# Optimization experiments

Hardware: AMD Instinct MI355X
Metric: run time of the kernel (lower is better)

## Reference

```python
import jax, jax.numpy as jnp
import numpy as np

COMMITMENT_COST = 0.25


def setup_inputs() -> dict:
    key = jax.random.key(0)
    k1, k2 = jax.random.split(key)
    B, H, W, D, K = 64, 32, 32, 64, 1024
    x = jax.random.normal(k1, (B, H, W, D), dtype=jnp.float32)
    # variance_scaling(fan_in=D, uniform) ~ U(-sqrt(3/D), sqrt(3/D)); plain normal*scale is fine for a reference
    embeddings = jax.random.uniform(k2, (D, K), dtype=jnp.float32,
                                    minval=-np.sqrt(3.0 / D), maxval=np.sqrt(3.0 / D))
    return {"x": x, "embeddings": embeddings}


def reference(x, embeddings):
    D = embeddings.shape[0]
    K = embeddings.shape[1]
    flat = x.reshape(-1, D)                                   # [N, D]
    # squared euclidean distance: ||f||^2 - 2 f.E + ||e||^2 -> [N, K]
    distance = (jnp.sum(flat ** 2, axis=1, keepdims=True)
                - 2.0 * jnp.matmul(flat, embeddings)
                + jnp.sum(embeddings ** 2, axis=0, keepdims=True))
    encoding_indices_flat = jnp.argmax(-distance, axis=1)     # [N]
    encodings = jax.nn.one_hot(encoding_indices_flat, K, dtype=distance.dtype)  # [N, K]
    encoding_indices = encoding_indices_flat.reshape(x.shape[:-1])
    # quantize: gather rows of E^T -> same shape as x
    quantized = jnp.take(embeddings.T, encoding_indices, axis=0)
    e_latent_loss = jnp.mean((jax.lax.stop_gradient(quantized) - x) ** 2)
    q_latent_loss = jnp.mean((quantized - jax.lax.stop_gradient(x)) ** 2)
    loss = q_latent_loss + COMMITMENT_COST * e_latent_loss
    quantized_st = x + jax.lax.stop_gradient(quantized - x)   # straight-through
    avg_probs = jnp.mean(encodings, axis=0)                   # [K]
    perplexity = jnp.exp(-jnp.sum(avg_probs * jnp.log(avg_probs + 1e-10)))
    return quantized_st, loss, perplexity, encoding_indices
```

## Files before the change

kernel.cpp:

```cpp
#include <hip/hip_runtime.h>
#include <math.h>


typedef __attribute__((ext_vector_type(8))) short short8v;
typedef __attribute__((ext_vector_type(4))) float float4v;
typedef unsigned short u16;
typedef unsigned int u32;

constexpr int D = 64;
constexpr int K = 1024;
constexpr int NPTS = 65536;
constexpr long QOFF = (long)NPTS * D;
constexpr float BIAS = 24.0f;
constexpr float GATE = 5e-3f;

constexpr size_t OFF_LOSS = 0;
constexpr size_t OFF_CNT  = 256;
constexpr size_t OFF_EC   = OFF_CNT + 4096;
constexpr size_t OFF_ECB  = OFF_EC + 4096;
constexpr size_t OFF_ET   = OFF_ECB + 4096;
constexpr size_t OFF_STG  = OFF_ET + (size_t)K * D * 4;

__device__ __forceinline__ float med3(float a, float b, float c) {
  return __builtin_amdgcn_fmed3f(a, b, c);
}
__device__ __forceinline__ u16 bf16rtn(float x) {
  u32 u = __float_as_uint(x);
  return (u16)((u + 0x7fffu + ((u >> 16) & 1u)) >> 16);
}
__device__ __forceinline__ float bf2f(u16 h) {
  return __uint_as_float(((u32)h) << 16);
}
__device__ __forceinline__ void gl_lds16(const void* g, void* l) {
  __builtin_amdgcn_global_load_lds(
      (const __attribute__((address_space(1))) u32*)g,
      (__attribute__((address_space(3))) u32*)l, 16, 0, 0);
}

__global__ __launch_bounds__(256) void vq_prep(const float* __restrict__ E,
                                               float* __restrict__ eC,
                                               float* __restrict__ eCb,
                                               float* __restrict__ Et,
                                               unsigned char* __restrict__ stg,
                                               double* __restrict__ lossSum,
                                               int* __restrict__ counts) {
  const int b = blockIdx.x;
  const int tid = threadIdx.x;
  if (b < 32) {
    int gid = b * 256 + tid;
    int k = gid & 1023;
    int g = gid >> 10;
    float v[8];
#pragma unroll
    for (int j = 0; j < 8; ++j) v[j] = E[(g * 8 + j) * K + k];
    *(float4*)&Et[(size_t)k * 64 + g * 8] = make_float4(v[0], v[1], v[2], v[3]);
    *(float4*)&Et[(size_t)k * 64 + g * 8 + 4] = make_float4(v[4], v[5], v[6], v[7]);
    short8v hv, lv;
#pragma unroll
    for (int j = 0; j < 8; ++j) {
      float m2 = -2.0f * v[j];
      u16 h = bf16rtn(m2);
      hv[j] = (short)h;
      lv[j] = (short)bf16rtn(m2 - bf2f(h));
    }
    size_t rowb = (size_t)(k >> 7) * 32768 + (size_t)(k & 127) * 256;
    int s = g >> 2, q = g & 3;
    int off = (s * 64 + q * 16) ^ ((k & 7) * 16);
    *(short8v*)&stg[rowb + off] = hv;
    *(short8v*)&stg[rowb + 128 + off] = lv;
  } else {
    int k = (b - 32) * 256 + tid;
    float c = __fmul_rn(E[k], E[k]);
#pragma unroll
    for (int d = 1; d < D; ++d) {
      float vv = E[d * K + k];
      c = __fadd_rn(c, __fmul_rn(vv, vv));
    }
    eC[k] = c;
    eCb[k] = c + BIAS;
    counts[k] = 0;
    if (k == 0) *lossSum = 0.0;
  }
}

__global__ __launch_bounds__(256) void vq_main(const float* __restrict__ x,
                                               const unsigned char* __restrict__ stg,
                                               const float* __restrict__ eC,
                                               const float* __restrict__ eCb,
                                               const float* __restrict__ Etg,
                                               float* __restrict__ out,
                                               double* __restrict__ lossSum,
                                               int* __restrict__ counts) {
  __shared__ __align__(16) unsigned char sbuf[2][32768];
  __shared__ __align__(16) float ecb[1024];
  __shared__ __align__(16) float topbuf[256 * 4];
  __shared__ int bkbuf[128];

  const int tid = threadIdx.x;
  const int w = tid >> 6;
  const int lane = tid & 63;
  const int col = lane & 15;
  const int quad = lane >> 4;
  const int blockBase = blockIdx.x * 128;
  const float INF = __builtin_inff();

  *(float4*)&ecb[tid * 4] = *(const float4*)&eCb[tid * 4];

  short8v Bh[2][2], Bl[2][2];
#pragma unroll
  for (int pt = 0; pt < 2; ++pt) {
    const float* xp = x + (size_t)(blockBase + w * 32 + pt * 16 + col) * 64;
#pragma unroll
    for (int s = 0; s < 2; ++s) {
      const float4* src = (const float4*)(xp + s * 32 + quad * 8);
      float4 a = src[0], b = src[1];
      float xs[8] = {a.x, a.y, a.z, a.w, b.x, b.y, b.z, b.w};
      short8v hf, lf;
#pragma unroll
      for (int j = 0; j < 8; ++j) {
        u16 h = bf16rtn(xs[j]);
        hf[j] = (short)h;
        lf[j] = (short)bf16rtn(xs[j] - bf2f(h));
      }
      Bh[pt][s] = hf;
      Bl[pt][s] = lf;
    }
  }

  {
    const unsigned char* s0 = stg + (size_t)tid * 16;
#pragma unroll
    for (int i = 0; i < 8; ++i)
      gl_lds16(s0 + i * 4096, &sbuf[0][tid * 16 + i * 4096]);
#pragma unroll
    for (int i = 0; i < 8; ++i)
      gl_lds16(s0 + 32768 + i * 4096, &sbuf[1][tid * 16 + i * 4096]);
  }
  asm volatile("s_waitcnt vmcnt(8) lgkmcnt(0)" ::: "memory");
  __builtin_amdgcn_s_barrier();
  __builtin_amdgcn_sched_barrier(0);
  asm volatile("" ::: "memory");

  float b1[2] = {INF, INF}, b2[2] = {INF, INF};
  const int swz = (col & 7) * 16;

#pragma unroll 1
  for (int ch = 0; ch < 8; ++ch) {
    unsigned char* bufB = sbuf[ch & 1];
#pragma unroll
    for (int ct = 0; ct < 8; ++ct) {
      const int rb = ct * 4096 + col * 256;
      short8v Ah0 = *(const short8v*)&bufB[rb + ((quad * 16) ^ swz)];
      short8v Ah1 = *(const short8v*)&bufB[rb + ((64 + quad * 16) ^ swz)];
      short8v Al0 = *(const short8v*)&bufB[rb + 128 + ((quad * 16) ^ swz)];
      short8v Al1 = *(const short8v*)&bufB[rb + 128 + ((64 + quad * 16) ^ swz)];
      float4v Ci = *(const float4v*)&ecb[ch * 128 + ct * 16 + quad * 4];
#pragma unroll
      for (int pt = 0; pt < 2; ++pt) {
        float4v Ca = Ci;
        float4v Cb = {0.f, 0.f, 0.f, 0.f};
        Ca = __builtin_amdgcn_mfma_f32_16x16x32_bf16(Ah0, Bh[pt][0], Ca, 0, 0, 0);
        Cb = __builtin_amdgcn_mfma_f32_16x16x32_bf16(Ah1, Bh[pt][1], Cb, 0, 0, 0);
        Ca = __builtin_amdgcn_mfma_f32_16x16x32_bf16(Al0, Bh[pt][0], Ca, 0, 0, 0);
        Cb = __builtin_amdgcn_mfma_f32_16x16x32_bf16(Al1, Bh[pt][1], Cb, 0, 0, 0);
        Ca = __builtin_amdgcn_mfma_f32_16x16x32_bf16(Ah0, Bl[pt][0], Ca, 0, 0, 0);
        Cb = __builtin_amdgcn_mfma_f32_16x16x32_bf16(Ah1, Bl[pt][1], Cb, 0, 0, 0);
#pragma unroll
        for (int r = 0; r < 4; ++r) {
          float dv = Ca[r] + Cb[r];
          u32 u = (__float_as_uint(dv) & 0xffffff00u) |
                  (u32)(ch * 32 + ct * 4 + r);
          float v = __uint_as_float(u);
          float pb = b1[pt];
          b1[pt] = fminf(pb, v);
          b2[pt] = med3(pb, b2[pt], v);
        }
      }
    }
    asm volatile("s_waitcnt lgkmcnt(0)" ::: "memory");
    __builtin_amdgcn_s_barrier();
    __builtin_amdgcn_sched_barrier(0);
    asm volatile("" ::: "memory");
    if (ch < 6) {
      const unsigned char* s2 = stg + (size_t)(ch + 2) * 32768 + (size_t)tid * 16;
#pragma unroll
      for (int i = 0; i < 8; ++i)
        gl_lds16(s2 + i * 4096, &bufB[tid * 16 + i * 4096]);
      asm volatile("s_waitcnt vmcnt(8)" ::: "memory");
    } else if (ch == 6) {
      asm volatile("s_waitcnt vmcnt(0)" ::: "memory");
    }
    if (ch < 7) {
      __builtin_amdgcn_s_barrier();
      __builtin_amdgcn_sched_barrier(0);
      asm volatile("" ::: "memory");
    }
  }

  topbuf[tid * 4 + 0] = b1[0];
  topbuf[tid * 4 + 1] = b2[0];
  topbuf[tid * 4 + 2] = b1[1];
  topbuf[tid * 4 + 3] = b2[1];
  __syncthreads();

  if (tid < 128) {
    const int mw = tid >> 5, mpt = (tid >> 4) & 1, mcol = tid & 15;
    float cv[8];
    int cq[8];
    float mv0 = INF, mv1 = INF;
    int q0 = 0;
#pragma unroll
    for (int q = 0; q < 4; ++q) {
      int lbase = (mw * 64 + q * 16 + mcol) * 4 + mpt * 2;
#pragma unroll
      for (int j = 0; j < 2; ++j) {
        float v = topbuf[lbase + j];
        cv[q * 2 + j] = v;
        cq[q * 2 + j] = q;
        if (v < mv0) { mv1 = mv0; mv0 = v; q0 = q; }
        else if (v < mv1) { mv1 = v; }
      }
    }
    u32 lb = __float_as_uint(mv0) & 255u;
    int bestk = (int)((lb >> 5) * 128 + ((lb >> 2) & 7) * 16 + q0 * 4 + (lb & 3));

    if (mv1 - mv0 < GATE) {
      const float* f = x + (size_t)(blockBase + tid) * 64;
      float r8[8];
#pragma unroll
      for (int j = 0; j < 8; ++j) { float fv = f[j]; r8[j] = __fmul_rn(fv, fv); }
#pragma unroll
      for (int i = 8; i < D; i += 8)
#pragma unroll
        for (int j = 0; j < 8; ++j) {
          float fv = f[i + j];
          r8[j] = __fadd_rn(r8[j], __fmul_rn(fv, fv));
        }
      float A = __fadd_rn(__fadd_rn(__fadd_rn(r8[0], r8[1]), __fadd_rn(r8[2], r8[3])),
                          __fadd_rn(__fadd_rn(r8[4], r8[5]), __fadd_rn(r8[6], r8[7])));
      float bd = INF;
      int bkk = K;
#pragma unroll
      for (int c = 0; c < 8; ++c) {
        u32 cb = __float_as_uint(cv[c]) & 255u;
        int k = (int)((cb >> 5) * 128 + ((cb >> 2) & 7) * 16 + cq[c] * 4 + (cb & 3));
        const float* er = Etg + (size_t)k * 64;
        float m = 0.f;
#pragma unroll
        for (int d = 0; d < D; ++d) m = __fmaf_rn(f[d], er[d], m);
        float dist = __fadd_rn(__fsub_rn(A, __fmul_rn(2.f, m)), eC[k]);
        bool better = (dist < bd) || (dist == bd && k < bkk);
        bd = better ? dist : bd;
        bkk = better ? k : bkk;
      }
      bestk = bkk;
    }

    bkbuf[tid] = bestk;
    out[QOFF + 2 + blockBase + tid] = (float)bestk;
    atomicAdd(&counts[bestk], 1);
  }
  __syncthreads();

  const int pp = tid >> 1, half = tid & 1;
  const int bk = bkbuf[pp];
  const float4* et = (const float4*)(Etg + (size_t)bk * 64 + half * 32);
  const float4* xr = (const float4*)(x + (size_t)(blockBase + pp) * 64 + half * 32);
  float4* ov = (float4*)(out + (size_t)(blockBase + pp) * 64 + half * 32);
  float errs = 0.f;
#pragma unroll
  for (int i = 0; i < 8; ++i) {
    float4 qv = et[i];
    float4 xv = xr[i];
    float dx;
    dx = qv.x - xv.x; errs = fmaf(dx, dx, errs);
    dx = qv.y - xv.y; errs = fmaf(dx, dx, errs);
    dx = qv.z - xv.z; errs = fmaf(dx, dx, errs);
    dx = qv.w - xv.w; errs = fmaf(dx, dx, errs);
    ov[i] = qv;
  }
  double de = (double)errs;
#pragma unroll
  for (int off = 32; off > 0; off >>= 1) de += __shfl_down(de, off, 64);
  if (lane == 0) atomicAdd(lossSum, de);
}

__global__ __launch_bounds__(256) void vq_finalize(const double* __restrict__ lossSum,
                                                   const int* __restrict__ counts,
                                                   float* __restrict__ out) {
  __shared__ double sh[256];
  double ent = 0.0;
  for (int k = threadIdx.x; k < K; k += 256) {
    double pp = (double)counts[k] / (double)NPTS;
    ent += pp * log(pp + 1e-10);
  }
  sh[threadIdx.x] = ent;
  __syncthreads();
  for (int s = 128; s > 0; s >>= 1) {
    if (threadIdx.x < s) sh[threadIdx.x] += sh[threadIdx.x + s];
    __syncthreads();
  }
  if (threadIdx.x == 0) {
    out[QOFF + 0] = (float)(1.25 * (*lossSum) / (double)((long)NPTS * D));
    out[QOFF + 1] = (float)exp(-sh[0]);
  }
}

extern "C" void kernel_launch(void* const* d_in, const int* in_sizes, int n_in,
                              void* d_out, int out_size, void* d_ws, size_t ws_size,
                              hipStream_t stream) {
  const float* x = (const float*)d_in[0];
  const float* E = (const float*)d_in[1];
  float* out = (float*)d_out;

  char* ws = (char*)d_ws;
  double* lossSum = (double*)(ws + OFF_LOSS);
  int* counts = (int*)(ws + OFF_CNT);
  float* eC = (float*)(ws + OFF_EC);
  float* eCb = (float*)(ws + OFF_ECB);
  float* Etg = (float*)(ws + OFF_ET);
  unsigned char* stgb = (unsigned char*)(ws + OFF_STG);

  vq_prep<<<36, 256, 0, stream>>>(E, eC, eCb, Etg, stgb, lossSum, counts);
  vq_main<<<NPTS / 128, 256, 0, stream>>>(x, stgb, eC, eCb, Etg, out,
                                          lossSum, counts);
  vq_finalize<<<1, 256, 0, stream>>>(lossSum, counts, out);
}
```

Before: 137.9 us.

## Give each wave private double-buffered codebook chunks to drop block barriers

Each of the four waves now streams the whole codebook into its own pair of 8 KB LDS buffers, in 32 small chunks instead of 8 shared 32 KB chunks. Waits use only per-wave vmcnt/lgkmcnt, so the block-wide s_barrier calls in the main loop go away and waves can drift independently. The trade is four times the global-to-LDS traffic per block, since every wave loads the full codebook. Index packing in the low mantissa bits and its decode are adjusted for the new chunk shape.

```diff
diff --git a/kernel.cpp b/kernel.cpp
--- a/kernel.cpp
+++ b/kernel.cpp
@@ -91,7 +91,7 @@
                                                float* __restrict__ out,
                                                double* __restrict__ lossSum,
                                                int* __restrict__ counts) {
-  __shared__ __align__(16) unsigned char sbuf[2][32768];
+  __shared__ __align__(16) unsigned char sbuf[4][2][8192];
   __shared__ __align__(16) float ecb[1024];
   __shared__ __align__(16) float topbuf[256 * 4];
   __shared__ int bkbuf[128];
@@ -128,15 +128,15 @@
   }
 
   {
-    const unsigned char* s0 = stg + (size_t)tid * 16;
+    const unsigned char* s0 = stg + (size_t)lane * 16;
 #pragma unroll
     for (int i = 0; i < 8; ++i)
-      gl_lds16(s0 + i * 4096, &sbuf[0][tid * 16 + i * 4096]);
+      gl_lds16(s0 + i * 1024, &sbuf[w][0][i * 1024 + lane * 16]);
 #pragma unroll
     for (int i = 0; i < 8; ++i)
-      gl_lds16(s0 + 32768 + i * 4096, &sbuf[1][tid * 16 + i * 4096]);
-  }
-  asm volatile("s_waitcnt vmcnt(8) lgkmcnt(0)" ::: "memory");
+      gl_lds16(s0 + 8192 + i * 1024, &sbuf[w][1][i * 1024 + lane * 16]);
+  }
+  asm volatile("s_waitcnt lgkmcnt(0)" ::: "memory");
   __builtin_amdgcn_s_barrier();
   __builtin_amdgcn_sched_barrier(0);
   asm volatile("" ::: "memory");
@@ -145,16 +145,21 @@
   const int swz = (col & 7) * 16;
 
 #pragma unroll 1
-  for (int ch = 0; ch < 8; ++ch) {
-    unsigned char* bufB = sbuf[ch & 1];
-#pragma unroll
-    for (int ct = 0; ct < 8; ++ct) {
-      const int rb = ct * 4096 + col * 256;
+  for (int ch = 0; ch < 32; ++ch) {
+    const unsigned char* bufB = sbuf[w][ch & 1];
+    if (ch < 31) {
+      asm volatile("s_waitcnt vmcnt(8)" ::: "memory");
+    } else {
+      asm volatile("s_waitcnt vmcnt(0)" ::: "memory");
+    }
+#pragma unroll
+    for (int ct2 = 0; ct2 < 2; ++ct2) {
+      const int rb = ct2 * 4096 + col * 256;
       short8v Ah0 = *(const short8v*)&bufB[rb + ((quad * 16) ^ swz)];
       short8v Ah1 = *(const short8v*)&bufB[rb + ((64 + quad * 16) ^ swz)];
       short8v Al0 = *(const short8v*)&bufB[rb + 128 + ((quad * 16) ^ swz)];
       short8v Al1 = *(const short8v*)&bufB[rb + 128 + ((64 + quad * 16) ^ swz)];
-      float4v Ci = *(const float4v*)&ecb[ch * 128 + ct * 16 + quad * 4];
+      float4v Ci = *(const float4v*)&ecb[ch * 32 + ct2 * 16 + quad * 4];
 #pragma unroll
       for (int pt = 0; pt < 2; ++pt) {
         float4v Ca = Ci;
@@ -169,7 +174,7 @@
         for (int r = 0; r < 4; ++r) {
           float dv = Ca[r] + Cb[r];
           u32 u = (__float_as_uint(dv) & 0xffffff00u) |
-                  (u32)(ch * 32 + ct * 4 + r);
+                  (u32)(ch * 8 + ct2 * 4 + r);
           float v = __uint_as_float(u);
           float pb = b1[pt];
           b1[pt] = fminf(pb, v);
@@ -178,22 +183,11 @@
       }
     }
     asm volatile("s_waitcnt lgkmcnt(0)" ::: "memory");
-    __builtin_amdgcn_s_barrier();
-    __builtin_amdgcn_sched_barrier(0);
-    asm volatile("" ::: "memory");
-    if (ch < 6) {
-      const unsigned char* s2 = stg + (size_t)(ch + 2) * 32768 + (size_t)tid * 16;
+    if (ch < 30) {
+      const unsigned char* s2 = stg + (size_t)(ch + 2) * 8192 + (size_t)lane * 16;
 #pragma unroll
       for (int i = 0; i < 8; ++i)
-        gl_lds16(s2 + i * 4096, &bufB[tid * 16 + i * 4096]);
-      asm volatile("s_waitcnt vmcnt(8)" ::: "memory");
-    } else if (ch == 6) {
-      asm volatile("s_waitcnt vmcnt(0)" ::: "memory");
-    }
-    if (ch < 7) {
-      __builtin_amdgcn_s_barrier();
-      __builtin_amdgcn_sched_barrier(0);
-      asm volatile("" ::: "memory");
+        gl_lds16(s2 + i * 1024, &sbuf[w][ch & 1][i * 1024 + lane * 16]);
     }
   }
 
@@ -222,7 +216,7 @@
       }
     }
     u32 lb = __float_as_uint(mv0) & 255u;
-    int bestk = (int)((lb >> 5) * 128 + ((lb >> 2) & 7) * 16 + q0 * 4 + (lb & 3));
+    int bestk = (int)((lb >> 3) * 32 + ((lb >> 2) & 1) * 16 + q0 * 4 + (lb & 3));
 
     if (mv1 - mv0 < GATE) {
       const float* f = x + (size_t)(blockBase + tid) * 64;
@@ -243,7 +237,7 @@
 #pragma unroll
       for (int c = 0; c < 8; ++c) {
         u32 cb = __float_as_uint(cv[c]) & 255u;
-        int k = (int)((cb >> 5) * 128 + ((cb >> 2) & 7) * 16 + cq[c] * 4 + (cb & 3));
+        int k = (int)((cb >> 3) * 32 + ((cb >> 2) & 1) * 16 + cq[c] * 4 + (cb & 3));
         const float* er = Etg + (size_t)k * 64;
         float m = 0.f;
 #pragma unroll
```

Result: faster. 129.4 us (-6.2%).
